# Optimization experiments

Hardware: AMD Instinct MI355X
Metric: run time of the kernel (lower is better)

## Reference

```python
import jax, jax.numpy as jnp
import numpy as np

EPS = 1e-12  # F.normalize default eps


def setup_inputs() -> dict:
    key = jax.random.key(0)
    k1, k2, k3, k4 = jax.random.split(key, 4)
    B, N, C, NH = 8, 4096, 512, 8
    x = jax.random.normal(k1, (B, N, C), dtype=jnp.float32)
    Wqkv = jax.random.normal(k2, (3 * C, C), dtype=jnp.float32) * 0.02
    Wproj = jax.random.normal(k3, (C, C), dtype=jnp.float32) * 0.02
    bproj = jax.random.normal(k4, (C,), dtype=jnp.float32) * 0.01
    temp = jnp.ones((NH, 1, 1), dtype=jnp.float32)
    return {"x": x, "Wqkv": Wqkv, "Wproj": Wproj, "bproj": bproj,
            "temp": temp, "H": 64, "W": 64}


def _l2norm(t):
    # normalize along last axis, matching F.normalize(p=2, eps=1e-12)
    return t / jnp.maximum(jnp.linalg.norm(t, axis=-1, keepdims=True), EPS)


def reference(x, Wqkv, Wproj, bproj, temp, H, W):
    B, N, C = x.shape
    nh = temp.shape[0]
    hd = C // nh
    # qkv projection: [B, N, 3, nh, hd]
    qkv = jnp.einsum('bnc,dc->bnd', x, Wqkv).reshape(B, N, 3, nh, hd)
    q = qkv[:, :, 0]  # [B, N, nh, hd]
    k = qkv[:, :, 1]
    v = qkv[:, :, 2]
    # transpose to [B, nh, hd, N] and L2-normalize along tokens (N)
    qn = _l2norm(q.transpose(0, 2, 3, 1))
    kn = _l2norm(k.transpose(0, 2, 3, 1))
    vt = v.transpose(0, 2, 3, 1)  # [B, nh, hd, N]
    # channel attention: [B, nh, hd, hd], scaled by learned per-head temp
    attn = jax.nn.softmax(jnp.einsum('bhcn,bhdn->bhcd', qn, kn) * temp, axis=-1)
    # [B, nh, hd, N] -> [B, N, nh, hd] -> [B, N, C]
    out = jnp.einsum('bhcd,bhdn->bhcn', attn, vt).transpose(0, 3, 1, 2).reshape(B, N, C)
    return jnp.einsum('bnc,dc->bnd', out, Wproj) + bproj
```

## Files before the change

### kernel.cpp

```cpp
#include <hip/hip_runtime.h>
#include <stdint.h>

#define DEVI __device__ __forceinline__

typedef __attribute__((ext_vector_type(8))) short bf16x8;
typedef __attribute__((ext_vector_type(4))) float f32x4;
typedef __attribute__((ext_vector_type(4))) unsigned short u16x4;
typedef __attribute__((ext_vector_type(4))) float float4v;

DEVI unsigned short f2bf(float f) {
  unsigned int u = __builtin_bit_cast(unsigned int, f);
  u += 0x7FFFu + ((u >> 16) & 1u);
  return (unsigned short)(u >> 16);
}
DEVI float bf2f(short s) {
  unsigned int u = ((unsigned int)(unsigned short)s) << 16;
  return __builtin_bit_cast(float, u);
}
DEVI void gload16(const unsigned short* g, unsigned short* l) {
  __builtin_amdgcn_global_load_lds(
      (const __attribute__((address_space(1))) unsigned int*)g,
      (__attribute__((address_space(3))) unsigned int*)l, 16, 0, 0);
}

__global__ void cast_prep(const float* __restrict__ x,
                          unsigned short* __restrict__ Xbf,
                          unsigned short* __restrict__ xT,
                          const float* __restrict__ Wqkv,
                          unsigned short* __restrict__ Wqk,
                          unsigned short* __restrict__ WvT) {
  __shared__ float tls[64][65];
  const int c = threadIdx.x & 63, rb = threadIdx.x >> 6;
  if (blockIdx.z < 8) {
    const int n0 = blockIdx.x * 64, c0 = blockIdx.y * 64, b = blockIdx.z;
#pragma unroll
    for (int rr = 0; rr < 16; ++rr) {
      int r = rb * 16 + rr;
      float v = x[((size_t)b * 4096 + n0 + r) * 512 + c0 + c];
      tls[r][c] = v;
      Xbf[((size_t)b * 4096 + n0 + r) * 512 + c0 + c] = f2bf(v);
    }
    __syncthreads();
#pragma unroll
    for (int rr = 0; rr < 16; ++rr) {
      int j = rb * 16 + rr;
      xT[((size_t)b * 512 + c0 + j) * 4096 + n0 + c] = f2bf(tls[c][j]);
    }
    return;
  }
  const int id = blockIdx.y * 64 + blockIdx.x;
  if (id < 256) {
    const float4v* src = (const float4v*)Wqkv;
    u16x4* dst = (u16x4*)Wqk;
    int base = id * 512 + threadIdx.x;
#pragma unroll
    for (int j = 0; j < 2; ++j) {
      int i = base + j * 256;
      float4v f = src[i];
      u16x4 o;
      o.x = f2bf(f.x); o.y = f2bf(f.y); o.z = f2bf(f.z); o.w = f2bf(f.w);
      dst[i] = o;
    }
  } else if (id < 320) {
    const int tile = id - 256;
    const int tr = tile >> 3, tc = tile & 7;
#pragma unroll
    for (int rr = 0; rr < 16; ++rr) {
      int r = rb * 16 + rr;
      tls[r][c] = Wqkv[(size_t)(1024 + tr * 64 + r) * 512 + tc * 64 + c];
    }
    __syncthreads();
#pragma unroll
    for (int rr = 0; rr < 16; ++rr) {
      int j = rb * 16 + rr;
      WvT[(size_t)(tc * 64 + j) * 512 + tr * 64 + c] = f2bf(tls[c][j]);
    }
  }
}

template <int KITERS>
DEVI void gemm_db(const unsigned short* gA, int strideA,
                  const unsigned short* gB, int strideB,
                  unsigned short (*lA)[4096], unsigned short (*lB)[4096],
                  int wave, int wr, int wc, int fr, int kg, f32x4 acc[4][4]) {
  const int wo = wave * 512;
#define STAGE_T(buf, kk)                                                    \
  gload16(gA + (kk) * 32, lA[buf] + wo);                                    \
  gload16(gA + (kk) * 32 + (size_t)64 * strideA, lA[buf] + wo + 2048);      \
  gload16(gB + (kk) * 32, lB[buf] + wo);                                    \
  gload16(gB + (kk) * 32 + (size_t)64 * strideB, lB[buf] + wo + 2048);
  STAGE_T(0, 0);
  __syncthreads();
  int cur = 0;
  for (int kk = 1; kk <= KITERS; ++kk) {
    if (kk < KITERS) { STAGE_T(cur ^ 1, kk); }
    bf16x8 af[4], bfv[4];
#pragma unroll
    for (int mi = 0; mi < 4; ++mi)
      af[mi] = *(const bf16x8*)&lA[cur][(wr * 64 + mi * 16 + fr) * 32 + kg * 8];
#pragma unroll
    for (int ni = 0; ni < 4; ++ni)
      bfv[ni] = *(const bf16x8*)&lB[cur][(wc * 64 + ni * 16 + fr) * 32 + kg * 8];
#pragma unroll
    for (int mi = 0; mi < 4; ++mi)
#pragma unroll
      for (int ni = 0; ni < 4; ++ni)
        acc[mi][ni] = __builtin_amdgcn_mfma_f32_16x16x32_bf16(
            af[mi], bfv[ni], acc[mi][ni], 0, 0, 0);
    __syncthreads();
    cur ^= 1;
  }
#undef STAGE_T
}

__launch_bounds__(256)
__global__ void gsyrk(const unsigned short* __restrict__ xT,
                      float* __restrict__ Gpart) {
  __shared__ __align__(16) unsigned short lA[2][4096];
  __shared__ __align__(16) unsigned short lB[2][4096];
  static const int PTC[10] = {0, 0, 0, 0, 1, 1, 1, 2, 2, 3};
  static const int PTD[10] = {0, 1, 2, 3, 1, 2, 3, 2, 3, 3};
  const int tid = threadIdx.x, wave = tid >> 6, lane = tid & 63;
  const int wr = wave >> 1, wc = wave & 1, fr = lane & 15, kg = lane >> 4;
  const int tc = PTC[blockIdx.x], td = PTD[blockIdx.x];
  const int chunk = blockIdx.y, b = blockIdx.z;
  const unsigned short* xb = xT + (size_t)b * 512 * 4096 + chunk * 1024;
  f32x4 acc[4][4] = {};
  const int sRow = wave * 16 + (lane >> 2);
  const int sK = (lane & 3) * 8;
  gemm_db<32>(xb + (size_t)(tc * 128 + sRow) * 4096 + sK, 4096,
              xb + (size_t)(td * 128 + sRow) * 4096 + sK, 4096,
              lA, lB, wave, wr, wc, fr, kg, acc);
  float* Gp = Gpart + (size_t)(chunk * 8 + b) * 512 * 512;
#pragma unroll
  for (int mi = 0; mi < 4; ++mi) {
    const int rIT = wr * 64 + mi * 16 + kg * 4;
#pragma unroll
    for (int ni = 0; ni < 4; ++ni) {
      const int cIT = wc * 64 + ni * 16 + fr;
      f32x4 v = acc[mi][ni];
#pragma unroll
      for (int r = 0; r < 4; ++r)
        Gp[(size_t)(tc * 128 + rIT + r) * 512 + td * 128 + cIT] = v[r];
      if (tc != td)
        *(f32x4*)&Gp[(size_t)(td * 128 + cIT) * 512 + tc * 128 + rIT] = v;
    }
  }
}

__global__ void greduce(const float* __restrict__ Gpart,
                        unsigned short* __restrict__ Gbf) {
  const int stride = gridDim.x * blockDim.x;
  const int n4 = 8 * 512 * 512 / 4;
  for (int i = blockIdx.x * blockDim.x + threadIdx.x; i < n4; i += stride) {
    float4v s = ((const float4v*)Gpart)[i];
#pragma unroll
    for (int c = 1; c < 4; ++c) {
      float4v t = ((const float4v*)(Gpart + (size_t)c * 8 * 512 * 512))[i];
      s.x += t.x; s.y += t.y; s.z += t.z; s.w += t.w;
    }
    u16x4 o;
    o.x = f2bf(s.x); o.y = f2bf(s.y); o.z = f2bf(s.z); o.w = f2bf(s.w);
    ((u16x4*)Gbf)[i] = o;
  }
}

__launch_bounds__(256)
__global__ void tall_gemm(const unsigned short* __restrict__ Wqk,
                          const unsigned short* __restrict__ Gbf,
                          unsigned short* __restrict__ Tbf,
                          float* __restrict__ ssPart) {
  __shared__ __align__(16) unsigned short lA[2][4096];
  __shared__ __align__(16) unsigned short lB[2][4096];
  __shared__ float ssL[128][2];
  const int tid = threadIdx.x, wave = tid >> 6, lane = tid & 63;
  const int wr = wave >> 1, wc = wave & 1, fr = lane & 15, kg = lane >> 4;
  const int rowBase = blockIdx.x * 128, colBase = blockIdx.y * 128;
  const int b = blockIdx.z;
  const unsigned short* Gb = Gbf + (size_t)b * 512 * 512;
  f32x4 acc[4][4] = {};
  const int sRow = wave * 16 + (lane >> 2);
  const int sK = (lane & 3) * 8;
  gemm_db<16>(Wqk + (size_t)(rowBase + sRow) * 512 + sK, 512,
              Gb + (size_t)(colBase + sRow) * 512 + sK, 512,
              lA, lB, wave, wr, wc, fr, kg, acc);
  unsigned short* Tb = Tbf + (size_t)b * 1024 * 512;
#pragma unroll
  for (int mi = 0; mi < 4; ++mi) {
    const int rbase = rowBase + wr * 64 + mi * 16 + kg * 4;
    f32x4 sacc = {0.f, 0.f, 0.f, 0.f};
#pragma unroll
    for (int ni = 0; ni < 4; ++ni) {
      const int col = colBase + wc * 64 + ni * 16 + fr;
      f32x4 v = acc[mi][ni];
#pragma unroll
      for (int r = 0; r < 4; ++r) {
        float w = bf2f((short)Wqk[(size_t)(rbase + r) * 512 + col]);
        Tb[(size_t)(rbase + r) * 512 + col] = f2bf(v[r]);
        sacc[r] += v[r] * w;
      }
    }
#pragma unroll
    for (int o = 1; o < 16; o <<= 1) {
#pragma unroll
      for (int r = 0; r < 4; ++r) sacc[r] += __shfl_xor(sacc[r], o);
    }
    if (fr == 0) {
#pragma unroll
      for (int r = 0; r < 4; ++r)
        ssL[wr * 64 + mi * 16 + kg * 4 + r][wc] = sacc[r];
    }
  }
  __syncthreads();
  if (tid < 128)
    ssPart[((size_t)blockIdx.y * 8 + b) * 1024 + rowBase + tid] =
        ssL[tid][0] + ssL[tid][1];
}

__global__ void s_softmax(const unsigned short* __restrict__ Tbf,
                          const unsigned short* __restrict__ Wqk,
                          const float* __restrict__ ssPart,
                          const float* __restrict__ temp,
                          float* __restrict__ attnOut) {
  __shared__ float Sl[64 * 64];
  __shared__ float invq[64], invk[64];
  const int bh = blockIdx.x, b = bh >> 3, h = bh & 7;
  const unsigned short* qbase = Tbf + (size_t)(b * 1024 + h * 64) * 512;
  const unsigned short* kbase = Wqk + (size_t)(512 + h * 64) * 512;
  const int t = threadIdx.x;
  const int wave = t >> 6, lane = t & 63;
  const int wr = wave >> 1, wc = wave & 1, fr = lane & 15, kg = lane >> 4;
  f32x4 acc[2][2] = {};
  for (int kk = 0; kk < 512; kk += 32) {
    bf16x8 a[2], bb[2];
#pragma unroll
    for (int mi = 0; mi < 2; ++mi)
      a[mi] = *(const bf16x8*)(qbase + (size_t)(wr * 32 + mi * 16 + fr) * 512 + kk + kg * 8);
#pragma unroll
    for (int ni = 0; ni < 2; ++ni)
      bb[ni] = *(const bf16x8*)(kbase + (size_t)(wc * 32 + ni * 16 + fr) * 512 + kk + kg * 8);
#pragma unroll
    for (int mi = 0; mi < 2; ++mi)
#pragma unroll
      for (int ni = 0; ni < 2; ++ni)
        acc[mi][ni] = __builtin_amdgcn_mfma_f32_16x16x32_bf16(a[mi], bb[ni], acc[mi][ni], 0, 0, 0);
  }
#pragma unroll
  for (int mi = 0; mi < 2; ++mi)
#pragma unroll
    for (int ni = 0; ni < 2; ++ni) {
      f32x4 v = acc[mi][ni];
#pragma unroll
      for (int r = 0; r < 4; ++r)
        Sl[(wr * 32 + mi * 16 + kg * 4 + r) * 64 + wc * 32 + ni * 16 + fr] = v[r];
    }
  if (t < 128) {
    const int r = (t >> 6) * 512 + h * 64 + (t & 63);
    float s = 0.f;
#pragma unroll
    for (int nt = 0; nt < 4; ++nt) s += ssPart[((size_t)nt * 8 + b) * 1024 + r];
    float inv = 1.f / fmaxf(sqrtf(s), 1e-12f);
    if (t < 64) invq[t] = inv;
    else invk[t - 64] = inv;
  }
  __syncthreads();
  const float tmp = temp[h];
  const int c = t >> 2, q4 = t & 3;
  float lg[16];
  float mx = -1e30f;
#pragma unroll
  for (int j = 0; j < 16; ++j) {
    const int d = q4 * 16 + j;
    lg[j] = Sl[c * 64 + d] * invq[c] * invk[d] * tmp;
    mx = fmaxf(mx, lg[j]);
  }
  mx = fmaxf(mx, __shfl_xor(mx, 1));
  mx = fmaxf(mx, __shfl_xor(mx, 2));
  float sum = 0.f;
#pragma unroll
  for (int j = 0; j < 16; ++j) {
    lg[j] = __expf(lg[j] - mx);
    sum += lg[j];
  }
  sum += __shfl_xor(sum, 1);
  sum += __shfl_xor(sum, 2);
  const float inv = 1.f / sum;
#pragma unroll
  for (int j = 0; j < 16; ++j)
    attnOut[(size_t)bh * 4096 + c * 64 + q4 * 16 + j] = lg[j] * inv;
}

__global__ void weff_kernel(const float* __restrict__ attn,
                            const float* __restrict__ Wproj,
                            unsigned short* __restrict__ Weff) {
  const int bh = blockIdx.x, eb = blockIdx.y;
  const int b = bh >> 3, h = bh & 7;
  __shared__ float at[64 * 64];
  for (int i = threadIdx.x; i < 4096; i += 256)
    at[i] = attn[(size_t)bh * 4096 + i];
  __syncthreads();
  const int e = eb * 64 + (threadIdx.x >> 2);
  const int dq = threadIdx.x & 3;
  float acc[16] = {};
  const float* wrow = Wproj + (size_t)e * 512 + h * 64;
  for (int c = 0; c < 64; ++c) {
    const float w = wrow[c];
#pragma unroll
    for (int j = 0; j < 16; ++j) acc[j] += w * at[c * 64 + dq * 16 + j];
  }
  unsigned short* outp = Weff + ((size_t)b * 512 + e) * 512 + h * 64 + dq * 16;
#pragma unroll
  for (int j = 0; j < 16; ++j) outp[j] = f2bf(acc[j]);
}

__launch_bounds__(256)
__global__ void wcomb_gemm(const unsigned short* __restrict__ WeffAll,
                           const unsigned short* __restrict__ WvT,
                           unsigned short* __restrict__ WcombAll) {
  __shared__ __align__(16) unsigned short lA[2][4096];
  __shared__ __align__(16) unsigned short lB[2][4096];
  const int tid = threadIdx.x, wave = tid >> 6, lane = tid & 63;
  const int wr = wave >> 1, wc = wave & 1, fr = lane & 15, kg = lane >> 4;
  const int b = blockIdx.z;
  const int rowBase = blockIdx.x * 128, colBase = blockIdx.y * 128;
  const unsigned short* A = WeffAll + (size_t)b * 512 * 512;
  f32x4 acc[4][4] = {};
  const int sRow = wave * 16 + (lane >> 2);
  const int sK = (lane & 3) * 8;
  gemm_db<16>(A + (size_t)(rowBase + sRow) * 512 + sK, 512,
              WvT + (size_t)(colBase + sRow) * 512 + sK, 512,
              lA, lB, wave, wr, wc, fr, kg, acc);
  unsigned short* Wc = WcombAll + (size_t)b * 512 * 512;
#pragma unroll
  for (int mi = 0; mi < 4; ++mi) {
    const int rbase = rowBase + wr * 64 + mi * 16 + kg * 4;
#pragma unroll
    for (int ni = 0; ni < 4; ++ni) {
      const int col = colBase + wc * 64 + ni * 16 + fr;
      f32x4 v = acc[mi][ni];
#pragma unroll
      for (int r = 0; r < 4; ++r)
        Wc[(size_t)(rbase + r) * 512 + col] = f2bf(v[r]);
    }
  }
}

__launch_bounds__(256)
__global__ void out_gemm(const unsigned short* __restrict__ Xbf,
                         const unsigned short* __restrict__ WcombAll,
                         const float* __restrict__ bias,
                         float* __restrict__ out) {
  __shared__ __align__(16) unsigned short lA[2][4096];
  __shared__ __align__(16) unsigned short lB[2][4096];
  const int tid = threadIdx.x, wave = tid >> 6, lane = tid & 63;
  const int wr = wave >> 1, wc = wave & 1, fr = lane & 15, kg = lane >> 4;
  const int b = blockIdx.z;
  const int rowBase = blockIdx.x * 128, colBase = blockIdx.y * 128;
  const unsigned short* A = Xbf + (size_t)b * 4096 * 512;
  const unsigned short* Bw = WcombAll + (size_t)b * 512 * 512;
  f32x4 acc[4][4] = {};
  const int sRow = wave * 16 + (lane >> 2);
  const int sK = (lane & 3) * 8;
  gemm_db<16>(A + (size_t)(rowBase + sRow) * 512 + sK, 512,
              Bw + (size_t)(colBase + sRow) * 512 + sK, 512,
              lA, lB, wave, wr, wc, fr, kg, acc);
#pragma unroll
  for (int mi = 0; mi < 4; ++mi) {
    const int rbase = rowBase + wr * 64 + mi * 16 + kg * 4;
#pragma unroll
    for (int ni = 0; ni < 4; ++ni) {
      const int col = colBase + wc * 64 + ni * 16 + fr;
      const float bcol = bias[col];
      f32x4 v = acc[mi][ni];
#pragma unroll
      for (int r = 0; r < 4; ++r)
        out[((size_t)b * 4096 + rbase + r) * 512 + col] = v[r] + bcol;
    }
  }
}

extern "C" void kernel_launch(void* const* d_in, const int* in_sizes, int n_in,
                              void* d_out, int out_size, void* d_ws, size_t ws_size,
                              hipStream_t stream) {
  const float* x = (const float*)d_in[0];
  const float* Wqkv = (const float*)d_in[1];
  const float* Wproj = (const float*)d_in[2];
  const float* bproj = (const float*)d_in[3];
  const float* temp = (const float*)d_in[4];
  float* out = (float*)d_out;

  char* ws = (char*)d_ws;
  unsigned short* Xbf = (unsigned short*)(ws + 0);
  unsigned short* xT = (unsigned short*)(ws + 33554432);
  unsigned short* Wqk = (unsigned short*)(ws + 67108864);
  unsigned short* WvT = (unsigned short*)(ws + 68157440);
  float* Gpart = (float*)(ws + 68681728);
  unsigned short* Gbf = (unsigned short*)(ws + 102236160);
  unsigned short* Tbf = (unsigned short*)(ws + 106430464);
  float* ssPart = (float*)(ws + 114819072);
  float* attn = (float*)(ws + 114950144);
  unsigned short* Weff = (unsigned short*)(ws + 115998720);
  unsigned short* Wcomb = (unsigned short*)(ws + 120193024);

  cast_prep<<<dim3(64, 8, 9), 256, 0, stream>>>(x, Xbf, xT, Wqkv, Wqk, WvT);
  gsyrk<<<dim3(10, 4, 8), 256, 0, stream>>>(xT, Gpart);
  greduce<<<1024, 256, 0, stream>>>(Gpart, Gbf);
  tall_gemm<<<dim3(8, 4, 8), 256, 0, stream>>>(Wqk, Gbf, Tbf, ssPart);
  s_softmax<<<64, 256, 0, stream>>>(Tbf, Wqk, ssPart, temp, attn);
  weff_kernel<<<dim3(64, 8), 256, 0, stream>>>(attn, Wproj, Weff);
  wcomb_gemm<<<dim3(4, 4, 8), 256, 0, stream>>>(Weff, WvT, Wcomb);
  out_gemm<<<dim3(32, 4, 8), 256, 0, stream>>>(Xbf, Wcomb, bproj, out);
}
```

Measured before the change: 142.3 us.

## Vectorize cast/transpose prep, split Gram SYRK finer with bf16 partials

The cast/transpose kernel now handles 128-token tiles with float4 loads and 16-byte bf16 stores for the transposed copy, and the Wqkv weight work is remapped onto the smaller grid. The Gram SYRK splits the token dimension into 8 chunks instead of 4, which doubles the block count for better occupancy. Its partial results are now stored as bf16 instead of fp32, which cuts partial-buffer traffic, and the reduce kernel sums 8 bf16 partials. Rounding each partial to bf16 before summation adds precision loss in the Gram matrix.

```diff
diff --git a/kernel.cpp b/kernel.cpp
--- a/kernel.cpp
+++ b/kernel.cpp
@@ -29,30 +29,42 @@
                           const float* __restrict__ Wqkv,
                           unsigned short* __restrict__ Wqk,
                           unsigned short* __restrict__ WvT) {
-  __shared__ float tls[64][65];
-  const int c = threadIdx.x & 63, rb = threadIdx.x >> 6;
+  __shared__ float tls[64 * 129];
+  const int t = threadIdx.x;
   if (blockIdx.z < 8) {
-    const int n0 = blockIdx.x * 64, c0 = blockIdx.y * 64, b = blockIdx.z;
-#pragma unroll
-    for (int rr = 0; rr < 16; ++rr) {
-      int r = rb * 16 + rr;
-      float v = x[((size_t)b * 4096 + n0 + r) * 512 + c0 + c];
-      tls[r][c] = v;
-      Xbf[((size_t)b * 4096 + n0 + r) * 512 + c0 + c] = f2bf(v);
+    const int n0 = blockIdx.x * 128, c0 = blockIdx.y * 64, b = blockIdx.z;
+    const int q = t & 15;
+    const int nl = t >> 4;
+#pragma unroll
+    for (int i = 0; i < 8; ++i) {
+      const int n = i * 16 + nl;
+      const size_t gi = ((size_t)b * 4096 + n0 + n) * 512 + c0 + q * 4;
+      float4v f = *(const float4v*)&x[gi];
+      u16x4 o;
+      o.x = f2bf(f.x); o.y = f2bf(f.y); o.z = f2bf(f.z); o.w = f2bf(f.w);
+      *(u16x4*)&Xbf[gi] = o;
+      tls[(q * 4 + 0) * 129 + n] = f.x;
+      tls[(q * 4 + 1) * 129 + n] = f.y;
+      tls[(q * 4 + 2) * 129 + n] = f.z;
+      tls[(q * 4 + 3) * 129 + n] = f.w;
     }
     __syncthreads();
-#pragma unroll
-    for (int rr = 0; rr < 16; ++rr) {
-      int j = rb * 16 + rr;
-      xT[((size_t)b * 512 + c0 + j) * 4096 + n0 + c] = f2bf(tls[c][j]);
+    const int cr = t >> 2, nq = t & 3;
+#pragma unroll
+    for (int ii = 0; ii < 4; ++ii) {
+      const int n = nq * 8 + ii * 32;
+      bf16x8 o;
+#pragma unroll
+      for (int s = 0; s < 8; ++s) o[s] = (short)f2bf(tls[cr * 129 + n + s]);
+      *(bf16x8*)&xT[((size_t)b * 512 + c0 + cr) * 4096 + n0 + n] = o;
     }
     return;
   }
-  const int id = blockIdx.y * 64 + blockIdx.x;
-  if (id < 256) {
+  const int id = blockIdx.y * 32 + blockIdx.x;
+  {
     const float4v* src = (const float4v*)Wqkv;
     u16x4* dst = (u16x4*)Wqk;
-    int base = id * 512 + threadIdx.x;
+    int base = id * 512 + t;
 #pragma unroll
     for (int j = 0; j < 2; ++j) {
       int i = base + j * 256;
@@ -61,19 +73,21 @@
       o.x = f2bf(f.x); o.y = f2bf(f.y); o.z = f2bf(f.z); o.w = f2bf(f.w);
       dst[i] = o;
     }
-  } else if (id < 320) {
-    const int tile = id - 256;
-    const int tr = tile >> 3, tc = tile & 7;
+  }
+  if (id < 64) {
+    const int tr = id >> 3, tc = id & 7;
+    const int c = t & 63, rb = t >> 6;
+    __syncthreads();
 #pragma unroll
     for (int rr = 0; rr < 16; ++rr) {
       int r = rb * 16 + rr;
-      tls[r][c] = Wqkv[(size_t)(1024 + tr * 64 + r) * 512 + tc * 64 + c];
+      tls[r * 65 + c] = Wqkv[(size_t)(1024 + tr * 64 + r) * 512 + tc * 64 + c];
     }
     __syncthreads();
 #pragma unroll
     for (int rr = 0; rr < 16; ++rr) {
       int j = rb * 16 + rr;
-      WvT[(size_t)(tc * 64 + j) * 512 + tr * 64 + c] = f2bf(tls[c][j]);
+      WvT[(size_t)(tc * 64 + j) * 512 + tr * 64 + c] = f2bf(tls[c * 65 + j]);
     }
   }
 }
@@ -115,7 +129,7 @@
 
 __launch_bounds__(256)
 __global__ void gsyrk(const unsigned short* __restrict__ xT,
-                      float* __restrict__ Gpart) {
+                      unsigned short* __restrict__ Gpart) {
   __shared__ __align__(16) unsigned short lA[2][4096];
   __shared__ __align__(16) unsigned short lB[2][4096];
   static const int PTC[10] = {0, 0, 0, 0, 1, 1, 1, 2, 2, 3};
@@ -124,14 +138,14 @@
   const int wr = wave >> 1, wc = wave & 1, fr = lane & 15, kg = lane >> 4;
   const int tc = PTC[blockIdx.x], td = PTD[blockIdx.x];
   const int chunk = blockIdx.y, b = blockIdx.z;
-  const unsigned short* xb = xT + (size_t)b * 512 * 4096 + chunk * 1024;
+  const unsigned short* xb = xT + (size_t)b * 512 * 4096 + chunk * 512;
   f32x4 acc[4][4] = {};
   const int sRow = wave * 16 + (lane >> 2);
   const int sK = (lane & 3) * 8;
-  gemm_db<32>(xb + (size_t)(tc * 128 + sRow) * 4096 + sK, 4096,
+  gemm_db<16>(xb + (size_t)(tc * 128 + sRow) * 4096 + sK, 4096,
               xb + (size_t)(td * 128 + sRow) * 4096 + sK, 4096,
               lA, lB, wave, wr, wc, fr, kg, acc);
-  float* Gp = Gpart + (size_t)(chunk * 8 + b) * 512 * 512;
+  unsigned short* Gp = Gpart + (size_t)(chunk * 8 + b) * 512 * 512;
 #pragma unroll
   for (int mi = 0; mi < 4; ++mi) {
     const int rIT = wr * 64 + mi * 16 + kg * 4;
@@ -141,26 +155,31 @@
       f32x4 v = acc[mi][ni];
 #pragma unroll
       for (int r = 0; r < 4; ++r)
-        Gp[(size_t)(tc * 128 + rIT + r) * 512 + td * 128 + cIT] = v[r];
-      if (tc != td)
-        *(f32x4*)&Gp[(size_t)(td * 128 + cIT) * 512 + tc * 128 + rIT] = v;
-    }
-  }
-}
-
-__global__ void greduce(const float* __restrict__ Gpart,
+        Gp[(size_t)(tc * 128 + rIT + r) * 512 + td * 128 + cIT] = f2bf(v[r]);
+      if (tc != td) {
+        u16x4 o;
+        o.x = f2bf(v[0]); o.y = f2bf(v[1]); o.z = f2bf(v[2]); o.w = f2bf(v[3]);
+        *(u16x4*)&Gp[(size_t)(td * 128 + cIT) * 512 + tc * 128 + rIT] = o;
+      }
+    }
+  }
+}
+
+__global__ void greduce(const unsigned short* __restrict__ Gpart,
                         unsigned short* __restrict__ Gbf) {
   const int stride = gridDim.x * blockDim.x;
   const int n4 = 8 * 512 * 512 / 4;
   for (int i = blockIdx.x * blockDim.x + threadIdx.x; i < n4; i += stride) {
-    float4v s = ((const float4v*)Gpart)[i];
-#pragma unroll
-    for (int c = 1; c < 4; ++c) {
-      float4v t = ((const float4v*)(Gpart + (size_t)c * 8 * 512 * 512))[i];
-      s.x += t.x; s.y += t.y; s.z += t.z; s.w += t.w;
+    const int b = i >> 16, j4 = i & 65535;
+    float s0 = 0, s1 = 0, s2 = 0, s3 = 0;
+#pragma unroll
+    for (int c = 0; c < 8; ++c) {
+      u16x4 v = ((const u16x4*)Gpart)[(size_t)(c * 8 + b) * 65536 + j4];
+      s0 += bf2f((short)v.x); s1 += bf2f((short)v.y);
+      s2 += bf2f((short)v.z); s3 += bf2f((short)v.w);
     }
     u16x4 o;
-    o.x = f2bf(s.x); o.y = f2bf(s.y); o.z = f2bf(s.z); o.w = f2bf(s.w);
+    o.x = f2bf(s0); o.y = f2bf(s1); o.z = f2bf(s2); o.w = f2bf(s3);
     ((u16x4*)Gbf)[i] = o;
   }
 }
@@ -394,7 +413,7 @@
   unsigned short* xT = (unsigned short*)(ws + 33554432);
   unsigned short* Wqk = (unsigned short*)(ws + 67108864);
   unsigned short* WvT = (unsigned short*)(ws + 68157440);
-  float* Gpart = (float*)(ws + 68681728);
+  unsigned short* Gpart = (unsigned short*)(ws + 68681728);
   unsigned short* Gbf = (unsigned short*)(ws + 102236160);
   unsigned short* Tbf = (unsigned short*)(ws + 106430464);
   float* ssPart = (float*)(ws + 114819072);
@@ -402,8 +421,8 @@
   unsigned short* Weff = (unsigned short*)(ws + 115998720);
   unsigned short* Wcomb = (unsigned short*)(ws + 120193024);
 
-  cast_prep<<<dim3(64, 8, 9), 256, 0, stream>>>(x, Xbf, xT, Wqkv, Wqk, WvT);
-  gsyrk<<<dim3(10, 4, 8), 256, 0, stream>>>(xT, Gpart);
+  cast_prep<<<dim3(32, 8, 9), 256, 0, stream>>>(x, Xbf, xT, Wqkv, Wqk, WvT);
+  gsyrk<<<dim3(10, 8, 8), 256, 0, stream>>>(xT, Gpart);
   greduce<<<1024, 256, 0, stream>>>(Gpart, Gbf);
   tall_gemm<<<dim3(8, 4, 8), 256, 0, stream>>>(Wqk, Gbf, Tbf, ssPart);
   s_softmax<<<64, 256, 0, stream>>>(Tbf, Wqk, ssPart, temp, attn);
```

After: 143.0 us. About the same (+0.5%).
